# Kernel tuning notes

Measured on AMD Instinct MI355X. Metric: run time of the kernel, lower is better.

## Reference

```python
import jax, jax.numpy as jnp
import numpy as np

N_NODES = 50000
N_EDGES = 800000
BN_EPS = 1e-5


def setup_inputs() -> dict:
    key = jax.random.key(0)
    ks = jax.random.split(key, 8)
    feat = jax.random.normal(ks[0], (N_NODES, 512), dtype=jnp.float32)
    src = jax.random.randint(ks[1], (N_EDGES,), 0, N_NODES, dtype=jnp.int32)
    dst = jax.random.randint(ks[2], (N_EDGES,), 0, N_NODES, dtype=jnp.int32)
    W0 = jax.random.normal(ks[3], (512, 128), dtype=jnp.float32) * 0.05
    W1 = jax.random.normal(ks[4], (128, 128), dtype=jnp.float32) * 0.05
    Wp1 = jax.random.normal(ks[5], (128, 256), dtype=jnp.float32) * 0.05
    bp1 = jnp.zeros((256,), dtype=jnp.float32)
    gamma = jnp.ones((256,), dtype=jnp.float32)
    beta = jnp.zeros((256,), dtype=jnp.float32)
    Wp2 = jax.random.normal(ks[6], (256, 128), dtype=jnp.float32) * 0.05
    bp2 = jnp.zeros((128,), dtype=jnp.float32)
    return {"feat": feat, "src": src, "dst": dst, "W0": W0, "W1": W1,
            "Wp1": Wp1, "bp1": bp1, "gamma": gamma, "beta": beta,
            "Wp2": Wp2, "bp2": bp2}


def reference(feat, src, dst, W0, W1, Wp1, bp1, gamma, beta, Wp2, bp2):
    N = feat.shape[0]
    # in-degrees, clamped to >=1, then D^{-1/2}
    deg = jax.ops.segment_sum(jnp.ones_like(dst, dtype=jnp.float32), dst,
                              num_segments=N)
    dinv = jnp.power(jnp.maximum(deg, 1.0), -0.5)[:, None]  # [N,1]

    def low_conv(h):
        # 2h - L_sym h = h + D^{-1/2} A D^{-1/2} h
        scaled = h * dinv
        agg = jax.ops.segment_sum(scaled[src], dst, num_segments=N)
        return h + agg * dinv

    h = low_conv(feat @ W0)      # linear0 (no bias) + conv0
    h = low_conv(h @ W1)         # linear1 (no bias) + conv1

    # MLPHead: Linear -> BatchNorm1d (training stats) -> ReLU -> Linear
    z = h @ Wp1 + bp1
    mu = jnp.mean(z, axis=0)
    var = jnp.mean((z - mu) ** 2, axis=0)  # biased var, torch training mode
    z = (z - mu) * jax.lax.rsqrt(var + BN_EPS) * gamma + beta
    z = jax.nn.relu(z)
    return z @ Wp2 + bp2
```

## Files before the change

kernel.cpp:

```cpp
#include <hip/hip_runtime.h>
#include <math.h>

constexpr int NN  = 50000;
constexpr int NE  = 800000;
constexpr int NNP = 50048;
constexpr int NB  = (NN + 255) / 256;

typedef __bf16 bf16x8 __attribute__((ext_vector_type(8)));
typedef float  f32x4  __attribute__((ext_vector_type(4)));
typedef __attribute__((address_space(1))) unsigned int as1_uint;
typedef __attribute__((address_space(3))) unsigned int as3_uint;

__device__ __forceinline__ unsigned short f2bf(float x) {
    unsigned int u = __float_as_uint(x);
    return (unsigned short)((u + 0x7FFFu + ((u >> 16) & 1u)) >> 16);
}
__device__ __forceinline__ float bf2f(unsigned short h) {
    return __uint_as_float(((unsigned int)h) << 16);
}
__device__ __forceinline__ float rdlanef(float v, int j) {
    return __uint_as_float(__builtin_amdgcn_readlane(__float_as_uint(v), j));
}

__device__ __forceinline__ void gload16(const unsigned short* g, unsigned short* l) {
    __builtin_amdgcn_global_load_lds((const as1_uint*)(unsigned long long)g,
                                     (as3_uint*)(unsigned long long)l, 16, 0, 0);
}

__global__ void k_count(const int* __restrict__ dst, int* __restrict__ cnt) {
    int i = blockIdx.x * blockDim.x + threadIdx.x;
    if (i < NE) atomicAdd(&cnt[dst[i]], 1);
}

__global__ void k_bsum(const int* __restrict__ cnt, int* __restrict__ bsum) {
    int i = blockIdx.x * 256 + threadIdx.x;
    int v = (i < NN) ? cnt[i] : 0;
#pragma unroll
    for (int off = 32; off; off >>= 1) v += __shfl_down(v, off, 64);
    __shared__ int tmp[4];
    if ((threadIdx.x & 63) == 0) tmp[threadIdx.x >> 6] = v;
    __syncthreads();
    if (threadIdx.x == 0) bsum[blockIdx.x] = tmp[0] + tmp[1] + tmp[2] + tmp[3];
}

__global__ void k_scan_bsum(const int* __restrict__ bsum, int* __restrict__ boff) {
    __shared__ int s[256];
    int t = threadIdx.x;
    int v = (t < NB) ? bsum[t] : 0;
    s[t] = v;
    __syncthreads();
    for (int off = 1; off < 256; off <<= 1) {
        int u = (t >= off) ? s[t - off] : 0;
        __syncthreads();
        s[t] += u;
        __syncthreads();
    }
    if (t < NB) boff[t] = s[t] - v;
}

__global__ void k_scan_block(const int* __restrict__ cnt, const int* __restrict__ boff,
                             int* __restrict__ rowoff, float* __restrict__ dinv) {
    __shared__ int s[256];
    int t = threadIdx.x;
    int i = blockIdx.x * 256 + t;
    int v = (i < NN) ? cnt[i] : 0;
    s[t] = v;
    __syncthreads();
    for (int off = 1; off < 256; off <<= 1) {
        int u = (t >= off) ? s[t - off] : 0;
        __syncthreads();
        s[t] += u;
        __syncthreads();
    }
    if (i < NN) {
        rowoff[i] = boff[blockIdx.x] + s[t] - v;
        dinv[i] = rsqrtf(fmaxf((float)v, 1.0f));
    }
}

__global__ void k_fill(const int* __restrict__ src, const int* __restrict__ dst,
                       const int* __restrict__ rowoff, int* __restrict__ cursor,
                       int* __restrict__ eidx) {
    int e = blockIdx.x * blockDim.x + threadIdx.x;
    if (e < NE) {
        int d = dst[e];
        int p = atomicAdd(&cursor[d], 1);
        eidx[rowoff[d] + p] = src[e];
    }
}

__global__ __launch_bounds__(256) void k_gather_shfl(
    const unsigned short* __restrict__ HH, const float* __restrict__ dinv,
    const int* __restrict__ rowoff, const int* __restrict__ cnt,
    const int* __restrict__ eidx, unsigned short* __restrict__ OH)
{
    int node = blockIdx.x * 4 + (threadIdx.x >> 6);
    int lane = threadIdx.x & 63;
    if (node >= NNP) return;
    size_t rb = (size_t)node * 128 + lane * 2;
    if (node >= NN) {
        *reinterpret_cast<ushort2*>(&OH[rb]) = make_ushort2(0, 0);
        return;
    }
    int beg = rowoff[node], n = cnt[node];
    int c2 = lane * 2;
    float ax = 0.f, ay = 0.f;
    for (int jj = 0; jj < n; jj += 64) {
        int m = min(n - jj, 64);
        int el = (lane < m) ? eidx[beg + jj + lane] : 0;
        float dl = dinv[el];
        int j = 0;
        for (; j + 8 <= m; j += 8) {
            int s0 = __builtin_amdgcn_readlane(el, j);
            int s1 = __builtin_amdgcn_readlane(el, j + 1);
            int s2 = __builtin_amdgcn_readlane(el, j + 2);
            int s3 = __builtin_amdgcn_readlane(el, j + 3);
            int s4 = __builtin_amdgcn_readlane(el, j + 4);
            int s5 = __builtin_amdgcn_readlane(el, j + 5);
            int s6 = __builtin_amdgcn_readlane(el, j + 6);
            int s7 = __builtin_amdgcn_readlane(el, j + 7);
            ushort2 v0 = *reinterpret_cast<const ushort2*>(&HH[(size_t)s0 * 128 + c2]);
            ushort2 v1 = *reinterpret_cast<const ushort2*>(&HH[(size_t)s1 * 128 + c2]);
            ushort2 v2 = *reinterpret_cast<const ushort2*>(&HH[(size_t)s2 * 128 + c2]);
            ushort2 v3 = *reinterpret_cast<const ushort2*>(&HH[(size_t)s3 * 128 + c2]);
            ushort2 v4 = *reinterpret_cast<const ushort2*>(&HH[(size_t)s4 * 128 + c2]);
            ushort2 v5 = *reinterpret_cast<const ushort2*>(&HH[(size_t)s5 * 128 + c2]);
            ushort2 v6 = *reinterpret_cast<const ushort2*>(&HH[(size_t)s6 * 128 + c2]);
            ushort2 v7 = *reinterpret_cast<const ushort2*>(&HH[(size_t)s7 * 128 + c2]);
            float d0 = rdlanef(dl, j),     d1 = rdlanef(dl, j + 1);
            float d2 = rdlanef(dl, j + 2), d3 = rdlanef(dl, j + 3);
            float d4 = rdlanef(dl, j + 4), d5 = rdlanef(dl, j + 5);
            float d6 = rdlanef(dl, j + 6), d7 = rdlanef(dl, j + 7);
            ax = fmaf(bf2f(v0.x), d0, ax); ay = fmaf(bf2f(v0.y), d0, ay);
            ax = fmaf(bf2f(v1.x), d1, ax); ay = fmaf(bf2f(v1.y), d1, ay);
            ax = fmaf(bf2f(v2.x), d2, ax); ay = fmaf(bf2f(v2.y), d2, ay);
            ax = fmaf(bf2f(v3.x), d3, ax); ay = fmaf(bf2f(v3.y), d3, ay);
            ax = fmaf(bf2f(v4.x), d4, ax); ay = fmaf(bf2f(v4.y), d4, ay);
            ax = fmaf(bf2f(v5.x), d5, ax); ay = fmaf(bf2f(v5.y), d5, ay);
            ax = fmaf(bf2f(v6.x), d6, ax); ay = fmaf(bf2f(v6.y), d6, ay);
            ax = fmaf(bf2f(v7.x), d7, ax); ay = fmaf(bf2f(v7.y), d7, ay);
        }
        for (; j < m; ++j) {
            int s0 = __builtin_amdgcn_readlane(el, j);
            float d0 = rdlanef(dl, j);
            ushort2 v0 = *reinterpret_cast<const ushort2*>(&HH[(size_t)s0 * 128 + c2]);
            ax = fmaf(bf2f(v0.x), d0, ax); ay = fmaf(bf2f(v0.y), d0, ay);
        }
    }
    float d = dinv[node];
    ushort2 sh = *reinterpret_cast<const ushort2*>(&HH[rb]);
    float hx = fmaf(ax, d, bf2f(sh.x));
    float hy = fmaf(ay, d, bf2f(sh.y));
    *reinterpret_cast<ushort2*>(&OH[rb]) = make_ushort2(f2bf(hx), f2bf(hy));
}

__global__ void k_wprep(const float* __restrict__ W0, const float* __restrict__ W1,
                        const float* __restrict__ Wp1, const float* __restrict__ Wp2,
                        unsigned short* __restrict__ W0t, unsigned short* __restrict__ W1pt,
                        unsigned short* __restrict__ Wp2t, float* __restrict__ stats) {
    int b = blockIdx.x, t = threadIdx.x;
    if (b < 128) {
        if (b < 2) stats[b * 256 + t] = 0.f;
        float s = 0.f;
        for (int k = 0; k < 128; ++k) s = fmaf(W1[b * 128 + k], Wp1[k * 256 + t], s);
        W1pt[t * 128 + b] = f2bf(s);
    } else if (b < 384) {
        int idx = (b - 128) * 256 + t;
        int k = idx >> 7, n = idx & 127;
        W0t[n * 512 + k] = f2bf(W0[idx]);
    } else {
        int idx = (b - 384) * 256 + t;
        int k = idx >> 7, n = idx & 127;
        Wp2t[n * 256 + k] = f2bf(Wp2[idx]);
    }
}

template <int K, int NCOLS, bool BIAS, int AMODE, int OMODE, bool STATS>
__global__ __launch_bounds__(512) void k_mfma(
    const unsigned short* __restrict__ AH, const float* __restrict__ Af,
    const unsigned short* __restrict__ BH, const float* __restrict__ bias,
    const float* __restrict__ stats, const float* __restrict__ gamma,
    const float* __restrict__ beta,
    float* __restrict__ C, unsigned short* __restrict__ OHs,
    float* __restrict__ statsOut)
{
    __shared__ __align__(16) unsigned short lds[2 * 4096];
    unsigned short* ldsA = lds;
    unsigned short* ldsB = lds + 4096;

    const int tid  = threadIdx.x;
    const int lane = tid & 63;
    const int wid  = tid >> 6;
    const int wm   = wid >> 1;
    const int wn   = wid & 1;
    const int row0 = blockIdx.x * 128;
    const int col0 = blockIdx.y * 128;

    const int srow  = tid >> 2;
    const int skg   = tid & 3;
    const int skswz = skg ^ ((srow >> 1) & 3);
    const size_t aSrc = (size_t)(row0 + srow) * K + skswz * 8;
    const size_t bSrc = (size_t)(col0 + srow) * K + skswz * 8;

    const int frow = lane & 15;
    const int fkg  = lane >> 4;

    __shared__ float s_scl[256], s_shf[256];
    if constexpr (AMODE == 2) {
        if (tid < K) {
            float mu  = stats[tid] * (1.0f / NN);
            float var = stats[256 + tid] * (1.0f / NN) - mu * mu;
            float s = gamma[tid] * rsqrtf(var + 1e-5f);
            s_scl[tid] = s;
            s_shf[tid] = beta[tid] - mu * s;
        }
        __syncthreads();
    }

    f32x4 acc[2][4] = {};

    for (int k0 = 0; k0 < K; k0 += 32) {
        if constexpr (AMODE == 1) {
            float4 f0, f1;
            if (row0 + srow < NN) {
                const float* ap = Af + aSrc + k0;
                f0 = *reinterpret_cast<const float4*>(ap);
                f1 = *reinterpret_cast<const float4*>(ap + 4);
            } else {
                f0 = make_float4(0.f, 0.f, 0.f, 0.f);
                f1 = f0;
            }
            uint4 w;
            w.x = (unsigned)f2bf(f0.x) | ((unsigned)f2bf(f0.y) << 16);
            w.y = (unsigned)f2bf(f0.z) | ((unsigned)f2bf(f0.w) << 16);
            w.z = (unsigned)f2bf(f1.x) | ((unsigned)f2bf(f1.y) << 16);
            w.w = (unsigned)f2bf(f1.z) | ((unsigned)f2bf(f1.w) << 16);
            *reinterpret_cast<uint4*>(&ldsA[tid * 8]) = w;
        } else if constexpr (AMODE == 2) {
            uint4 raw = *reinterpret_cast<const uint4*>(&AH[aSrc + k0]);
            unsigned rw[4] = {raw.x, raw.y, raw.z, raw.w};
            int kc = k0 + skswz * 8;
            float vv[8];
#pragma unroll
            for (int q = 0; q < 8; ++q) {
                float z = bf2f((unsigned short)((q & 1) ? (rw[q >> 1] >> 16)
                                                        : (rw[q >> 1] & 0xFFFF)));
                vv[q] = fmaxf(fmaf(z, s_scl[kc + q], s_shf[kc + q]), 0.f);
            }
            uint4 w;
            w.x = (unsigned)f2bf(vv[0]) | ((unsigned)f2bf(vv[1]) << 16);
            w.y = (unsigned)f2bf(vv[2]) | ((unsigned)f2bf(vv[3]) << 16);
            w.z = (unsigned)f2bf(vv[4]) | ((unsigned)f2bf(vv[5]) << 16);
            w.w = (unsigned)f2bf(vv[6]) | ((unsigned)f2bf(vv[7]) << 16);
            *reinterpret_cast<uint4*>(&ldsA[tid * 8]) = w;
        } else {
            gload16(AH + aSrc + k0, ldsA + tid * 8);
        }
        gload16(BH + bSrc + k0, ldsB + tid * 8);
        __syncthreads();

        bf16x8 a_h[2], b_h[4];
#pragma unroll
        for (int mi = 0; mi < 2; ++mi) {
            int ar  = wm * 32 + mi * 16 + frow;
            int idx = ar * 32 + ((fkg ^ ((ar >> 1) & 3)) * 8);
            a_h[mi] = *reinterpret_cast<const bf16x8*>(&ldsA[idx]);
        }
#pragma unroll
        for (int ni = 0; ni < 4; ++ni) {
            int bc  = wn * 64 + ni * 16 + frow;
            int idx = bc * 32 + ((fkg ^ ((bc >> 1) & 3)) * 8);
            b_h[ni] = *reinterpret_cast<const bf16x8*>(&ldsB[idx]);
        }
#pragma unroll
        for (int mi = 0; mi < 2; ++mi)
#pragma unroll
            for (int ni = 0; ni < 4; ++ni)
                acc[mi][ni] = __builtin_amdgcn_mfma_f32_16x16x32_bf16(a_h[mi], b_h[ni], acc[mi][ni], 0, 0, 0);
        __syncthreads();
    }

    float psum[4] = {0.f, 0.f, 0.f, 0.f}, psq[4] = {0.f, 0.f, 0.f, 0.f};
#pragma unroll
    for (int mi = 0; mi < 2; ++mi) {
        int rbase = row0 + wm * 32 + mi * 16 + (lane >> 4) * 4;
#pragma unroll
        for (int ni = 0; ni < 4; ++ni) {
            int col = col0 + wn * 64 + ni * 16 + (lane & 15);
            float b = BIAS ? bias[col] : 0.f;
#pragma unroll
            for (int r = 0; r < 4; ++r) {
                int row = rbase + r;
                float v = acc[mi][ni][r] + b;
                if constexpr (STATS) {
                    if (row < NN) { psum[ni] += v; psq[ni] = fmaf(v, v, psq[ni]); }
                }
                if constexpr (OMODE == 1) {
                    OHs[(size_t)row * NCOLS + col] = f2bf(v);
                } else {
                    if (row < NN) C[(size_t)row * NCOLS + col] = v;
                }
            }
        }
    }

    if constexpr (STATS) {
        __shared__ float s_sum[128], s_sq[128];
        if (tid < 128) { s_sum[tid] = 0.f; s_sq[tid] = 0.f; }
        __syncthreads();
#pragma unroll
        for (int ni = 0; ni < 4; ++ni) {
            float a = psum[ni], q = psq[ni];
            a += __shfl_xor(a, 16); a += __shfl_xor(a, 32);
            q += __shfl_xor(q, 16); q += __shfl_xor(q, 32);
            if ((lane >> 4) == 0) {
                int cl = wn * 64 + ni * 16 + lane;
                atomicAdd(&s_sum[cl], a);
                atomicAdd(&s_sq[cl], q);
            }
        }
        __syncthreads();
        if (tid < 128) {
            atomicAdd(&statsOut[col0 + tid], s_sum[tid]);
            atomicAdd(&statsOut[256 + col0 + tid], s_sq[tid]);
        }
    }
}

extern "C" void kernel_launch(void* const* d_in, const int* in_sizes, int n_in,
                              void* d_out, int out_size, void* d_ws, size_t ws_size,
                              hipStream_t stream) {
    const float* feat  = (const float*)d_in[0];
    const int*   src   = (const int*)d_in[1];
    const int*   dst   = (const int*)d_in[2];
    const float* W0    = (const float*)d_in[3];
    const float* W1    = (const float*)d_in[4];
    const float* Wp1   = (const float*)d_in[5];
    const float* bp1   = (const float*)d_in[6];
    const float* gamma = (const float*)d_in[7];
    const float* beta  = (const float*)d_in[8];
    const float* Wp2   = (const float*)d_in[9];
    const float* bp2   = (const float*)d_in[10];
    float* out = (float*)d_out;

    char* wsb = (char*)d_ws;
    float* dinv   = (float*)(wsb + 4ull * 0);
    int*   cnt    = (int*)  (wsb + 4ull * 50048);
    int*   cursor = (int*)  (wsb + 4ull * 100096);
    int*   rowoff = (int*)  (wsb + 4ull * 150144);
    int*   bsum   = (int*)  (wsb + 4ull * 200192);
    int*   boff   = (int*)  (wsb + 4ull * 200448);
    int*   eidx   = (int*)  (wsb + 4ull * 200704);
    float* stats  = (float*)(wsb + 4ull * 1000704);
    unsigned short* W0t  = (unsigned short*)(wsb + 4ull * 1034496);
    unsigned short* W1pt = W0t + 65536;
    unsigned short* Wp2t = W1pt + 32768;
    unsigned short* H0 = (unsigned short*)(wsb + 4ull * 1165568);
    unsigned short* h1 = (unsigned short*)(wsb + 4ull * 4368640);
    unsigned short* h2 = H0;
    unsigned short* ZH = (unsigned short*)(wsb + 4ull * 7571712);

    const int GX = NNP / 128;

    hipMemsetAsync(cnt, 0, 2 * 50048 * sizeof(int), stream);
    k_count<<<(NE + 255) / 256, 256, 0, stream>>>(dst, cnt);
    k_bsum<<<NB, 256, 0, stream>>>(cnt, bsum);
    k_scan_bsum<<<1, 256, 0, stream>>>(bsum, boff);
    k_scan_block<<<NB, 256, 0, stream>>>(cnt, boff, rowoff, dinv);
    k_fill<<<(NE + 255) / 256, 256, 0, stream>>>(src, dst, rowoff, cursor, eidx);

    k_wprep<<<512, 256, 0, stream>>>(W0, W1, Wp1, Wp2, W0t, W1pt, Wp2t, stats);

    k_mfma<512, 128, false, 1, 1, false><<<dim3(GX, 1), 512, 0, stream>>>(
        nullptr, feat, W0t, nullptr, nullptr, nullptr, nullptr,
        nullptr, H0, nullptr);

    k_gather_shfl<<<NNP / 4, 256, 0, stream>>>(H0, dinv, rowoff, cnt, eidx, h1);
    k_gather_shfl<<<NNP / 4, 256, 0, stream>>>(h1, dinv, rowoff, cnt, eidx, h2);

    k_mfma<128, 256, true, 0, 1, true><<<dim3(GX, 2), 512, 0, stream>>>(
        h2, nullptr, W1pt, bp1, nullptr, nullptr, nullptr,
        nullptr, ZH, stats);

    k_mfma<256, 128, true, 2, 0, false><<<dim3(GX, 1), 512, 0, stream>>>(
        ZH, nullptr, Wp2t, bp2, stats, gamma, beta,
        out, nullptr, nullptr);
}
```

Measured before the change: 237.7 us.

## Merge edge count into weight prep and CSR fill into first GEMM launch

The degree-count atomics now run as extra blocks of the weight-prep kernel. The CSR fill scatter runs as extra blocks appended to a dedicated first-layer GEMM kernel, so the latency-bound atomic work overlaps with compute-bound work and two launches are removed. The first GEMM is split out of the templated kernel into its own function. A risk is that the fill blocks share a launch-bounds-512 kernel with large LDS use, which may affect scheduling of the GEMM blocks.

```diff
diff --git a/kernel.cpp b/kernel.cpp
--- a/kernel.cpp
+++ b/kernel.cpp
@@ -5,6 +5,8 @@
 constexpr int NE  = 800000;
 constexpr int NNP = 50048;
 constexpr int NB  = (NN + 255) / 256;
+constexpr int GX  = NNP / 128;
+constexpr int FILLB = (NE + 511) / 512;
 
 typedef __bf16 bf16x8 __attribute__((ext_vector_type(8)));
 typedef float  f32x4  __attribute__((ext_vector_type(4)));
@@ -25,11 +27,6 @@
 __device__ __forceinline__ void gload16(const unsigned short* g, unsigned short* l) {
     __builtin_amdgcn_global_load_lds((const as1_uint*)(unsigned long long)g,
                                      (as3_uint*)(unsigned long long)l, 16, 0, 0);
-}
-
-__global__ void k_count(const int* __restrict__ dst, int* __restrict__ cnt) {
-    int i = blockIdx.x * blockDim.x + threadIdx.x;
-    if (i < NE) atomicAdd(&cnt[dst[i]], 1);
 }
 
 __global__ void k_bsum(const int* __restrict__ cnt, int* __restrict__ bsum) {
@@ -75,17 +72,6 @@
     if (i < NN) {
         rowoff[i] = boff[blockIdx.x] + s[t] - v;
         dinv[i] = rsqrtf(fmaxf((float)v, 1.0f));
-    }
-}
-
-__global__ void k_fill(const int* __restrict__ src, const int* __restrict__ dst,
-                       const int* __restrict__ rowoff, int* __restrict__ cursor,
-                       int* __restrict__ eidx) {
-    int e = blockIdx.x * blockDim.x + threadIdx.x;
-    if (e < NE) {
-        int d = dst[e];
-        int p = atomicAdd(&cursor[d], 1);
-        eidx[rowoff[d] + p] = src[e];
     }
 }
 
@@ -154,11 +140,17 @@
     *reinterpret_cast<ushort2*>(&OH[rb]) = make_ushort2(f2bf(hx), f2bf(hy));
 }
 
-__global__ void k_wprep(const float* __restrict__ W0, const float* __restrict__ W1,
-                        const float* __restrict__ Wp1, const float* __restrict__ Wp2,
-                        unsigned short* __restrict__ W0t, unsigned short* __restrict__ W1pt,
-                        unsigned short* __restrict__ Wp2t, float* __restrict__ stats) {
+__global__ void k_wprep_count(const float* __restrict__ W0, const float* __restrict__ W1,
+                              const float* __restrict__ Wp1, const float* __restrict__ Wp2,
+                              unsigned short* __restrict__ W0t, unsigned short* __restrict__ W1pt,
+                              unsigned short* __restrict__ Wp2t, float* __restrict__ stats,
+                              const int* __restrict__ dst, int* __restrict__ cnt) {
     int b = blockIdx.x, t = threadIdx.x;
+    if (b >= 512) {
+        int i = (b - 512) * 256 + t;
+        if (i < NE) atomicAdd(&cnt[dst[i]], 1);
+        return;
+    }
     if (b < 128) {
         if (b < 2) stats[b * 256 + t] = 0.f;
         float s = 0.f;
@@ -175,10 +167,101 @@
     }
 }
 
+__global__ __launch_bounds__(512) void k_gemm1_fill(
+    const float* __restrict__ Af, const unsigned short* __restrict__ BH,
+    unsigned short* __restrict__ OHs,
+    const int* __restrict__ src, const int* __restrict__ dst,
+    const int* __restrict__ rowoff, int* __restrict__ cursor, int* __restrict__ eidx)
+{
+    if (blockIdx.x >= GX) {
+        int e = (blockIdx.x - GX) * 512 + threadIdx.x;
+        if (e < NE) {
+            int d = dst[e];
+            int p = atomicAdd(&cursor[d], 1);
+            eidx[rowoff[d] + p] = src[e];
+        }
+        return;
+    }
+    constexpr int K = 512, NCOLS = 128;
+    __shared__ __align__(16) unsigned short lds[2 * 4096];
+    unsigned short* ldsA = lds;
+    unsigned short* ldsB = lds + 4096;
+
+    const int tid  = threadIdx.x;
+    const int lane = tid & 63;
+    const int wid  = tid >> 6;
+    const int wm   = wid >> 1;
+    const int wn   = wid & 1;
+    const int row0 = blockIdx.x * 128;
+
+    const int srow  = tid >> 2;
+    const int skg   = tid & 3;
+    const int skswz = skg ^ ((srow >> 1) & 3);
+    const size_t aSrc = (size_t)(row0 + srow) * K + skswz * 8;
+    const size_t bSrc = (size_t)srow * K + skswz * 8;
+
+    const int frow = lane & 15;
+    const int fkg  = lane >> 4;
+
+    f32x4 acc[2][4] = {};
+
+    for (int k0 = 0; k0 < K; k0 += 32) {
+        float4 f0, f1;
+        if (row0 + srow < NN) {
+            const float* ap = Af + aSrc + k0;
+            f0 = *reinterpret_cast<const float4*>(ap);
+            f1 = *reinterpret_cast<const float4*>(ap + 4);
+        } else {
+            f0 = make_float4(0.f, 0.f, 0.f, 0.f);
+            f1 = f0;
+        }
+        uint4 w;
+        w.x = (unsigned)f2bf(f0.x) | ((unsigned)f2bf(f0.y) << 16);
+        w.y = (unsigned)f2bf(f0.z) | ((unsigned)f2bf(f0.w) << 16);
+        w.z = (unsigned)f2bf(f1.x) | ((unsigned)f2bf(f1.y) << 16);
+        w.w = (unsigned)f2bf(f1.z) | ((unsigned)f2bf(f1.w) << 16);
+        *reinterpret_cast<uint4*>(&ldsA[tid * 8]) = w;
+        gload16(BH + bSrc + k0, ldsB + tid * 8);
+        __syncthreads();
+
+        bf16x8 a_h[2], b_h[4];
+#pragma unroll
+        for (int mi = 0; mi < 2; ++mi) {
+            int ar  = wm * 32 + mi * 16 + frow;
+            int idx = ar * 32 + ((fkg ^ ((ar >> 1) & 3)) * 8);
+            a_h[mi] = *reinterpret_cast<const bf16x8*>(&ldsA[idx]);
+        }
+#pragma unroll
+        for (int ni = 0; ni < 4; ++ni) {
+            int bc  = wn * 64 + ni * 16 + frow;
+            int idx = bc * 32 + ((fkg ^ ((bc >> 1) & 3)) * 8);
+            b_h[ni] = *reinterpret_cast<const bf16x8*>(&ldsB[idx]);
+        }
+#pragma unroll
+        for (int mi = 0; mi < 2; ++mi)
+#pragma unroll
+            for (int ni = 0; ni < 4; ++ni)
+                acc[mi][ni] = __builtin_amdgcn_mfma_f32_16x16x32_bf16(a_h[mi], b_h[ni], acc[mi][ni], 0, 0, 0);
+        __syncthreads();
+    }
+
+#pragma unroll
+    for (int mi = 0; mi < 2; ++mi) {
+        int rbase = row0 + wm * 32 + mi * 16 + (lane >> 4) * 4;
+#pragma unroll
+        for (int ni = 0; ni < 4; ++ni) {
+            int col = wn * 64 + ni * 16 + (lane & 15);
+#pragma unroll
+            for (int r = 0; r < 4; ++r)
+                OHs[(size_t)(rbase + r) * NCOLS + col] = f2bf(acc[mi][ni][r]);
+        }
+    }
+}
+
 template <int K, int NCOLS, bool BIAS, int AMODE, int OMODE, bool STATS>
 __global__ __launch_bounds__(512) void k_mfma(
-    const unsigned short* __restrict__ AH, const float* __restrict__ Af,
-    const unsigned short* __restrict__ BH, const float* __restrict__ bias,
+    const unsigned short* __restrict__ AH, const unsigned short* __restrict__ BH,
+    const float* __restrict__ bias,
     const float* __restrict__ stats, const float* __restrict__ gamma,
     const float* __restrict__ beta,
     float* __restrict__ C, unsigned short* __restrict__ OHs,
@@ -220,23 +303,7 @@
     f32x4 acc[2][4] = {};
 
     for (int k0 = 0; k0 < K; k0 += 32) {
-        if constexpr (AMODE == 1) {
-            float4 f0, f1;
-            if (row0 + srow < NN) {
-                const float* ap = Af + aSrc + k0;
-                f0 = *reinterpret_cast<const float4*>(ap);
-                f1 = *reinterpret_cast<const float4*>(ap + 4);
-            } else {
-                f0 = make_float4(0.f, 0.f, 0.f, 0.f);
-                f1 = f0;
-            }
-            uint4 w;
-            w.x = (unsigned)f2bf(f0.x) | ((unsigned)f2bf(f0.y) << 16);
-            w.y = (unsigned)f2bf(f0.z) | ((unsigned)f2bf(f0.w) << 16);
-            w.z = (unsigned)f2bf(f1.x) | ((unsigned)f2bf(f1.y) << 16);
-            w.w = (unsigned)f2bf(f1.z) | ((unsigned)f2bf(f1.w) << 16);
-            *reinterpret_cast<uint4*>(&ldsA[tid * 8]) = w;
-        } else if constexpr (AMODE == 2) {
+        if constexpr (AMODE == 2) {
             uint4 raw = *reinterpret_cast<const uint4*>(&AH[aSrc + k0]);
             unsigned rw[4] = {raw.x, raw.y, raw.z, raw.w};
             int kc = k0 + skswz * 8;
@@ -360,29 +427,22 @@
     unsigned short* h2 = H0;
     unsigned short* ZH = (unsigned short*)(wsb + 4ull * 7571712);
 
-    const int GX = NNP / 128;
-
     hipMemsetAsync(cnt, 0, 2 * 50048 * sizeof(int), stream);
-    k_count<<<(NE + 255) / 256, 256, 0, stream>>>(dst, cnt);
+    k_wprep_count<<<512 + (NE + 255) / 256, 256, 0, stream>>>(
+        W0, W1, Wp1, Wp2, W0t, W1pt, Wp2t, stats, dst, cnt);
     k_bsum<<<NB, 256, 0, stream>>>(cnt, bsum);
     k_scan_bsum<<<1, 256, 0, stream>>>(bsum, boff);
     k_scan_block<<<NB, 256, 0, stream>>>(cnt, boff, rowoff, dinv);
-    k_fill<<<(NE + 255) / 256, 256, 0, stream>>>(src, dst, rowoff, cursor, eidx);
-
-    k_wprep<<<512, 256, 0, stream>>>(W0, W1, Wp1, Wp2, W0t, W1pt, Wp2t, stats);
-
-    k_mfma<512, 128, false, 1, 1, false><<<dim3(GX, 1), 512, 0, stream>>>(
-        nullptr, feat, W0t, nullptr, nullptr, nullptr, nullptr,
-        nullptr, H0, nullptr);
+
+    k_gemm1_fill<<<GX + FILLB, 512, 0, stream>>>(
+        feat, W0t, H0, src, dst, rowoff, cursor, eidx);
 
     k_gather_shfl<<<NNP / 4, 256, 0, stream>>>(H0, dinv, rowoff, cnt, eidx, h1);
     k_gather_shfl<<<NNP / 4, 256, 0, stream>>>(h1, dinv, rowoff, cnt, eidx, h2);
 
     k_mfma<128, 256, true, 0, 1, true><<<dim3(GX, 2), 512, 0, stream>>>(
-        h2, nullptr, W1pt, bp1, nullptr, nullptr, nullptr,
-        nullptr, ZH, stats);
+        h2, W1pt, bp1, nullptr, nullptr, nullptr, nullptr, ZH, stats);
 
     k_mfma<256, 128, true, 2, 0, false><<<dim3(GX, 1), 512, 0, stream>>>(
-        ZH, nullptr, Wp2t, bp2, stats, gamma, beta,
-        out, nullptr, nullptr);
-}
+        ZH, Wp2t, bp2, stats, gamma, beta, out, nullptr, nullptr);
+}
```

New measurement: 215.8 us. -9.2%, faster.
